# Kernel optimization log

Hardware: AMD Instinct MI355X
Metric: run time of the kernel (lower is better)

Reference implementation:

```python
import jax, jax.numpy as jnp
import numpy as np
from jax.scipy.special import logsumexp

B, T, N = 512, 1024, 64


def setup_inputs() -> dict:
    key = jax.random.key(0)
    k1, k2, k3, k4, k5, k6 = jax.random.split(key, 6)
    emit = jax.random.normal(k1, (B, T, N), dtype=jnp.float32)
    target = jax.random.randint(k2, (B, T), 0, N)
    # valid monotone mask: each sequence has length in [T//2, T], length >= 1
    lengths = jax.random.randint(k3, (B,), T // 2, T + 1)
    mask = jnp.arange(T)[None, :] < lengths[:, None]  # [B, T] bool
    trans = 0.1 * jax.random.normal(k4, (N, N), dtype=jnp.float32)
    strans = 0.1 * jax.random.normal(k5, (N,), dtype=jnp.float32)
    etrans = 0.1 * jax.random.normal(k6, (N,), dtype=jnp.float32)
    return {"emit": emit, "target": target, "mask": mask,
            "trans": trans, "strans": strans, "etrans": etrans}


def _get_logZ(emit_t, mask_t, trans, strans, etrans):
    # emit_t: [T, B, N], mask_t: [T, B]
    alpha0 = strans[None, :] + emit_t[0]  # [B, N]

    def step(alpha, inp):
        e_i, m_i = inp  # [B, N], [B]
        # scores[b, j] = logsumexp_i(alpha[b, i] + trans[i, j] + e_i[b, j])
        scores = logsumexp(alpha[:, :, None] + trans[None, :, :], axis=1) + e_i
        alpha = jnp.where(m_i[:, None], scores, alpha)
        return alpha, None

    alpha, _ = jax.lax.scan(step, alpha0, (emit_t[1:], mask_t[1:]))
    logZ = logsumexp(alpha + etrans[None, :], axis=1).sum()
    return logZ / B


def _get_score(emit_t, target_t, mask_t, trans, strans, etrans):
    # emit_t: [T, B, N], target_t/mask_t: [T, B]
    emit_scores = jnp.take_along_axis(emit_t, target_t[:, :, None], axis=2)[:, :, 0]  # [T, B]
    trans_scores = trans[target_t[:-1], target_t[1:]]  # [T-1, B]
    scores = emit_scores.at[1:].add(trans_scores)
    score = jnp.where(mask_t, scores, 0.0).sum()
    ends = mask_t.sum(axis=0) - 1  # [B]
    score = score + strans[target_t[0]].sum()
    last_tags = target_t[ends, jnp.arange(target_t.shape[1])]
    score = score + etrans[last_tags].sum()
    return score / B


def reference(emit, target, mask, trans, strans, etrans):
    # batch_first=True -> move to time-major [T, B, ...]
    emit_t = jnp.swapaxes(emit, 0, 1)
    target_t = target.T
    mask_t = mask.T
    logZ = _get_logZ(emit_t, mask_t, trans, strans, etrans)
    score = _get_score(emit_t, target_t, mask_t, trans, strans, etrans)
    return logZ - score
```

## Files before the change

kernel.cpp:

```cpp
#include <hip/hip_runtime.h>

#define Bn 512
#define Tn 1024
#define Nn 64
#define BURN 16
#define NBUF 3

typedef float    f4  __attribute__((ext_vector_type(4)));
typedef __fp16   pk2 __attribute__((ext_vector_type(2)));
typedef __fp16   pk4 __attribute__((ext_vector_type(4)));
typedef __fp16   pk8 __attribute__((ext_vector_type(8)));
typedef _Float16 h8v __attribute__((ext_vector_type(8)));

typedef __attribute__((address_space(1))) void as1_void;
typedef __attribute__((address_space(3))) void as3_void;

__device__ __forceinline__ void stage16(const float* g, float* l) {
    __builtin_amdgcn_global_load_lds((as1_void*)(unsigned long long)g,
                                     (as3_void*)(unsigned long long)l, 16, 0, 0);
}
#define VMCNT(N) asm volatile("s_waitcnt vmcnt(" #N ")" ::: "memory")

__device__ __forceinline__ float wave_sum(float v) {
#pragma unroll
    for (int off = 32; off >= 1; off >>= 1) v += __shfl_xor(v, off, 64);
    return v;
}

__global__ __launch_bounds__(64) void crf_mfma(
    const float* __restrict__ emit,
    const int*   __restrict__ target,
    const int*   __restrict__ mask,
    const float* __restrict__ trans,
    const float* __restrict__ strans,
    const float* __restrict__ etrans,
    float*       __restrict__ out)
{
    __shared__ __align__(16) float sbuf[NBUF * 4096];

    const int lane = threadIdx.x;
    const int n = lane & 15;
    const int g = lane >> 4;
    const int b = blockIdx.x;
    const size_t ebase = (size_t)b * Tn * Nn;

    h8v A[4][2];
#pragma unroll
    for (int r = 0; r < 4; ++r)
#pragma unroll
        for (int hh = 0; hh < 2; ++hh) {
            h8v a;
#pragma unroll
            for (int j = 0; j < 8; ++j) {
                int kk = 32 * hh + 16 * (j >> 2) + 4 * g + (j & 3);
                a[j] = (_Float16)__expf(trans[kk * Nn + 16 * r + n]);
            }
            A[r][hh] = a;
        }

    const int* mrow = mask + (size_t)b * Tn;
    int lsum = 0;
#pragma unroll
    for (int k = 0; k < Tn / Nn; ++k) lsum += mrow[k * Nn + lane];
#pragma unroll
    for (int off = 32; off >= 1; off >>= 1) lsum += __shfl_xor(lsum, off, 64);
    const int len = lsum;

    int startc[16];
#pragma unroll
    for (int c = 0; c < 16; ++c) {
        int a = ((c * len) >> 4) - BURN;
        startc[c] = (a < 1) ? 1 : a;
    }
    const int a0v   = (n * len) >> 4;
    const int start = startc[n];
    const int tendv = (((n + 1) * len) >> 4) - 1;
    const int maxk  = ((len + 15) >> 4) + BURN;

    float wsel[4][4];
#pragma unroll
    for (int r = 0; r < 4; ++r) {
        f4 ee = *(const f4*)(emit + ebase + (size_t)(len - 1) * Nn + 16 * r + 4 * g);
        f4 et = *(const f4*)(etrans + 16 * r + 4 * g);
#pragma unroll
        for (int c = 0; c < 4; ++c)
            wsel[r][c] = (n == 15) ? __expf(ee[c] + et[c]) : 1.0f;
    }

    float U[4][4];
#pragma unroll
    for (int r = 0; r < 4; ++r) {
        f4 st = *(const f4*)(strans + 16 * r + 4 * g);
#pragma unroll
        for (int c = 0; c < 4; ++c)
            U[r][c] = (start == 1) ? __expf(st[c]) : 1.0f;
    }

    int   S = 0;
    float L0 = 0.0f, contrib = 0.0f;

    const int rowoff = lane >> 4;
    const int fb     = 4 * (lane & 15);
    auto stage = [&](int bf, int jgrp) {
        float* lb = sbuf + bf * 4096;
#pragma unroll
        for (int cc = 0; cc < 16; ++cc) {
            int row = startc[cc] + 4 * jgrp - 1 + rowoff;
            if (row > Tn - 1) row = Tn - 1;
            int fs = (fb + (64 - 4 * cc)) & 63;
            stage16(emit + ebase + (size_t)row * Nn + fs, lb + cc * 256);
        }
    };

    VMCNT(0);
    stage(0, 0); stage(1, 1);
    __builtin_amdgcn_sched_barrier(0);

    const f4 zero4 = {0.f, 0.f, 0.f, 0.f};
    const int ngrp = (maxk + 3) >> 2;
    const int ro = (4 * g + 4 * n) & 63;
    int bc = 0, bs = 2;

    for (int jg = 0; jg < ngrp; ++jg) {
        stage(bs, jg + 2);
        VMCNT(32);
        __builtin_amdgcn_sched_barrier(0);
        const float* cb = sbuf + bc * 4096 + n * 256;

#pragma unroll
        for (int q = 0; q < 4; ++q) {
            const int k = 4 * jg + q;

            const float* sb = cb + q * 64;
            f4 w0 = *(const f4*)(sb + ((ro +  0) & 63));
            f4 w1 = *(const f4*)(sb + ((ro + 16) & 63));
            f4 w2 = *(const f4*)(sb + ((ro + 32) & 63));
            f4 w3 = *(const f4*)(sb + ((ro + 48) & 63));
            float Wx[4][4];
#pragma unroll
            for (int c = 0; c < 4; ++c) {
                Wx[0][c] = __expf(w0[c]);
                Wx[1][c] = __expf(w1[c]);
                Wx[2][c] = __expf(w2[c]);
                Wx[3][c] = __expf(w3[c]);
            }

            bool br = n && ((start + k) == a0v);
            if (__any(br)) {
                float cs = 0.f;
#pragma unroll
                for (int r = 0; r < 4; ++r)
#pragma unroll
                    for (int c = 0; c < 4; ++c) cs += U[r][c];
                cs += __shfl_xor(cs, 16, 64);
                cs += __shfl_xor(cs, 32, 64);
                float l0v = __logf(cs);
                if (br) { L0 = l0v; S = 0; }
            }

            float m0 = fmaxf(fmaxf(U[0][0], U[0][1]), fmaxf(U[0][2], U[0][3]));
            float m1 = fmaxf(fmaxf(U[1][0], U[1][1]), fmaxf(U[1][2], U[1][3]));
            float m2 = fmaxf(fmaxf(U[2][0], U[2][1]), fmaxf(U[2][2], U[2][3]));
            float m3 = fmaxf(fmaxf(U[3][0], U[3][1]), fmaxf(U[3][2], U[3][3]));
            float mx = fmaxf(fmaxf(m0, m1), fmaxf(m2, m3));
            mx = fmaxf(mx, __shfl_xor(mx, 16, 64));
            mx = fmaxf(mx, __shfl_xor(mx, 32, 64));
            const int mk = 127 - ((__float_as_int(mx) >> 23) & 0xff);
            S += mk;
            const float sc2 = __int_as_float((127 + mk) << 23);

            float P_[4][4];
#pragma unroll
            for (int r = 0; r < 4; ++r)
#pragma unroll
                for (int c = 0; c < 4; ++c) P_[r][c] = U[r][c] * sc2 * Wx[r][c];

            pk2 c00 = __builtin_amdgcn_cvt_pkrtz(P_[0][0], P_[0][1]);
            pk2 c01 = __builtin_amdgcn_cvt_pkrtz(P_[0][2], P_[0][3]);
            pk2 c10 = __builtin_amdgcn_cvt_pkrtz(P_[1][0], P_[1][1]);
            pk2 c11 = __builtin_amdgcn_cvt_pkrtz(P_[1][2], P_[1][3]);
            pk2 c20 = __builtin_amdgcn_cvt_pkrtz(P_[2][0], P_[2][1]);
            pk2 c21 = __builtin_amdgcn_cvt_pkrtz(P_[2][2], P_[2][3]);
            pk2 c30 = __builtin_amdgcn_cvt_pkrtz(P_[3][0], P_[3][1]);
            pk2 c31 = __builtin_amdgcn_cvt_pkrtz(P_[3][2], P_[3][3]);
            pk4 b0lo = __builtin_shufflevector(c00, c01, 0, 1, 2, 3);
            pk4 b0hi = __builtin_shufflevector(c10, c11, 0, 1, 2, 3);
            pk4 b1lo = __builtin_shufflevector(c20, c21, 0, 1, 2, 3);
            pk4 b1hi = __builtin_shufflevector(c30, c31, 0, 1, 2, 3);
            pk8 b0p = __builtin_shufflevector(b0lo, b0hi, 0, 1, 2, 3, 4, 5, 6, 7);
            pk8 b1p = __builtin_shufflevector(b1lo, b1hi, 0, 1, 2, 3, 4, 5, 6, 7);
            h8v B0 = __builtin_bit_cast(h8v, b0p);
            h8v B1 = __builtin_bit_cast(h8v, b1p);

#pragma unroll
            for (int r = 0; r < 4; ++r) {
                f4 acc = __builtin_amdgcn_mfma_f32_16x16x32_f16(A[r][0], B0, zero4, 0, 0, 0);
                acc     = __builtin_amdgcn_mfma_f32_16x16x32_f16(A[r][1], B1, acc,   0, 0, 0);
#pragma unroll
                for (int c = 0; c < 4; ++c) U[r][c] = acc[c];
            }

            bool rec = (start + k) == tendv;
            if (__any(rec)) {
                float cs = 0.f;
#pragma unroll
                for (int r = 0; r < 4; ++r)
#pragma unroll
                    for (int c = 0; c < 4; ++c) cs = fmaf(U[r][c], wsel[r][c], cs);
                cs += __shfl_xor(cs, 16, 64);
                cs += __shfl_xor(cs, 32, 64);
                float lv = __logf(cs);
                if (rec) contrib = lv - (float)S * 0.6931471805599453f - L0;
            }
        }
        bc = (bc == NBUF - 1) ? 0 : bc + 1;
        bs = (bs == NBUF - 1) ? 0 : bs + 1;
    }
    VMCNT(0);

    float tot = wave_sum(contrib) * 0.25f;

    const int* trow = target + (size_t)b * Tn;
    float sc = 0.0f;
#pragma unroll
    for (int k = 0; k < Tn / Nn; ++k) {
        int t = k * Nn + lane;
        if (t < len) {
            int gT = trow[t];
            sc += emit[ebase + (size_t)t * Nn + gT];
            if (t > 0) sc += trans[trow[t - 1] * Nn + gT];
        }
    }
    sc = wave_sum(sc);

    if (lane == 0) {
        sc += strans[trow[0]] + etrans[trow[len - 1]];
        atomicAdd(out, (tot - sc) * (1.0f / (float)Bn));
    }
}

extern "C" void kernel_launch(void* const* d_in, const int* in_sizes, int n_in,
                              void* d_out, int out_size, void* d_ws, size_t ws_size,
                              hipStream_t stream) {
    const float* emit   = (const float*)d_in[0];
    const int*   target = (const int*)d_in[1];
    const int*   mask   = (const int*)d_in[2];
    const float* trans  = (const float*)d_in[3];
    const float* strans = (const float*)d_in[4];
    const float* etrans = (const float*)d_in[5];
    float* out = (float*)d_out;

    (void)hipMemsetAsync(out, 0, sizeof(float), stream);
    crf_mfma<<<Bn, Nn, 0, stream>>>(emit, target, mask, trans, strans, etrans, out);
}
```

Measured before the change: 226.2 us.

## Split each sequence's time chunks across two blocks per batch element

Launches two blocks per batch element so each sequence is cut into 32 time chunks instead of 16, and each block handles 16 of them with burn-in. This halves the serial recurrence length per block and doubles the grid, giving more waves in flight to hide MFMA and exp latency. LDS buffering drops from triple to double buffering to reduce shared memory per block and allow more blocks per CU. The cost is more redundant burn-in work and a shallower prefetch pipeline.

Result: faster. 221.1 us (-2.2%).

```diff
diff --git a/kernel.cpp b/kernel.cpp
--- a/kernel.cpp
+++ b/kernel.cpp
@@ -3,8 +3,9 @@
 #define Bn 512
 #define Tn 1024
 #define Nn 64
+#define WB 2
 #define BURN 16
-#define NBUF 3
+#define NBUF 2
 
 typedef float    f4  __attribute__((ext_vector_type(4)));
 typedef __fp16   pk2 __attribute__((ext_vector_type(2)));
@@ -41,7 +42,9 @@
     const int lane = threadIdx.x;
     const int n = lane & 15;
     const int g = lane >> 4;
-    const int b = blockIdx.x;
+    const int b = blockIdx.x & (Bn - 1);
+    const int h = blockIdx.x >> 9;
+    const int m = 16 * h + n;
     const size_t ebase = (size_t)b * Tn * Nn;
 
     h8v A[4][2];
@@ -68,14 +71,14 @@
 
     int startc[16];
 #pragma unroll
-    for (int c = 0; c < 16; ++c) {
-        int a = ((c * len) >> 4) - BURN;
-        startc[c] = (a < 1) ? 1 : a;
-    }
-    const int a0v   = (n * len) >> 4;
+    for (int cc = 0; cc < 16; ++cc) {
+        int a = (((16 * h + cc) * len) >> 5) - BURN;
+        startc[cc] = (a < 1) ? 1 : a;
+    }
+    const int a0v   = (m * len) >> 5;
     const int start = startc[n];
-    const int tendv = (((n + 1) * len) >> 4) - 1;
-    const int maxk  = ((len + 15) >> 4) + BURN;
+    const int tendv = (((m + 1) * len) >> 5) - 1;
+    const int maxk  = ((len + 31) >> 5) + BURN;
 
     float wsel[4][4];
 #pragma unroll
@@ -84,7 +87,7 @@
         f4 et = *(const f4*)(etrans + 16 * r + 4 * g);
 #pragma unroll
         for (int c = 0; c < 4; ++c)
-            wsel[r][c] = (n == 15) ? __expf(ee[c] + et[c]) : 1.0f;
+            wsel[r][c] = (m == 31) ? __expf(ee[c] + et[c]) : 1.0f;
     }
 
     float U[4][4];
@@ -113,19 +116,18 @@
     };
 
     VMCNT(0);
-    stage(0, 0); stage(1, 1);
+    stage(0, 0);
     __builtin_amdgcn_sched_barrier(0);
 
     const f4 zero4 = {0.f, 0.f, 0.f, 0.f};
     const int ngrp = (maxk + 3) >> 2;
     const int ro = (4 * g + 4 * n) & 63;
-    int bc = 0, bs = 2;
 
     for (int jg = 0; jg < ngrp; ++jg) {
-        stage(bs, jg + 2);
-        VMCNT(32);
+        stage((jg + 1) & 1, jg + 1);
+        VMCNT(16);
         __builtin_amdgcn_sched_barrier(0);
-        const float* cb = sbuf + bc * 4096 + n * 256;
+        const float* cb = sbuf + (jg & 1) * 4096 + n * 256;
 
 #pragma unroll
         for (int q = 0; q < 4; ++q) {
@@ -145,7 +147,7 @@
                 Wx[3][c] = __expf(w3[c]);
             }
 
-            bool br = n && ((start + k) == a0v);
+            bool br = m && ((start + k) == a0v);
             if (__any(br)) {
                 float cs = 0.f;
 #pragma unroll
@@ -213,29 +215,30 @@
                 if (rec) contrib = lv - (float)S * 0.6931471805599453f - L0;
             }
         }
-        bc = (bc == NBUF - 1) ? 0 : bc + 1;
-        bs = (bs == NBUF - 1) ? 0 : bs + 1;
     }
     VMCNT(0);
 
     float tot = wave_sum(contrib) * 0.25f;
 
+    float sc = 0.0f;
     const int* trow = target + (size_t)b * Tn;
-    float sc = 0.0f;
-#pragma unroll
-    for (int k = 0; k < Tn / Nn; ++k) {
-        int t = k * Nn + lane;
-        if (t < len) {
-            int gT = trow[t];
-            sc += emit[ebase + (size_t)t * Nn + gT];
-            if (t > 0) sc += trans[trow[t - 1] * Nn + gT];
-        }
-    }
-    sc = wave_sum(sc);
+    if (h == 0) {
+#pragma unroll
+        for (int k = 0; k < Tn / Nn; ++k) {
+            int t = k * Nn + lane;
+            if (t < len) {
+                int gT = trow[t];
+                sc += emit[ebase + (size_t)t * Nn + gT];
+                if (t > 0) sc += trans[trow[t - 1] * Nn + gT];
+            }
+        }
+        sc = wave_sum(sc);
+    }
 
     if (lane == 0) {
-        sc += strans[trow[0]] + etrans[trow[len - 1]];
-        atomicAdd(out, (tot - sc) * (1.0f / (float)Bn));
+        float add = tot;
+        if (h == 0) add -= sc + strans[trow[0]] + etrans[trow[len - 1]];
+        atomicAdd(out, add * (1.0f / (float)Bn));
     }
 }
 
@@ -251,5 +254,5 @@
     float* out = (float*)d_out;
 
     (void)hipMemsetAsync(out, 0, sizeof(float), stream);
-    crf_mfma<<<Bn, Nn, 0, stream>>>(emit, target, mask, trans, strans, etrans, out);
-}
+    crf_mfma<<<Bn * WB, Nn, 0, stream>>>(emit, target, mask, trans, strans, etrans, out);
+}
```
